# Kernel tuning notes

Hardware: AMD Instinct MI355X
Metric: run time of the kernel (lower is better)

Reference implementation:

```python
import jax, jax.numpy as jnp
import numpy as np

B, NPG = 128, 128          # graphs, nodes per graph
N = B * NPG                # total nodes
K = 16                     # kNN neighbors within cutoff
D = 256                    # embedding_depth
H, DH = 4, 32              # heads = num_layers, head dim = (D//2)//H
L = 4                      # num graph convolutions
NR = 50                    # num_radial
CUTOFF = 2.0
OUT = 3 + 100              # 3 + max_ntypes


def setup_inputs() -> dict:
    rng = np.random.default_rng(0)
    pos = rng.standard_normal((N, 3)).astype(np.float32)
    nbrs = np.zeros((N, K), np.int32)
    mask = np.zeros((N, K), np.float32)
    for g in range(B):  # per-graph kNN with radial cutoff (setup only, numpy)
        p = pos[g * NPG:(g + 1) * NPG]
        d2 = ((p[:, None, :] - p[None, :, :]) ** 2).sum(-1)
        np.fill_diagonal(d2, np.inf)
        idx = np.argsort(d2, axis=1)[:, :K]
        dk = np.sqrt(np.take_along_axis(d2, idx, 1))
        nbrs[g * NPG:(g + 1) * NPG] = idx + g * NPG
        mask[g * NPG:(g + 1) * NPG] = (dk <= CUTOFF).astype(np.float32)
    batch_idx = np.repeat(np.arange(B, dtype=np.int32), NPG)

    key = jax.random.key(0)
    ks = jax.random.split(key, 12)
    s = 0.02
    return {
        'encoding': jax.random.normal(ks[0], (B, D), jnp.float32),
        'pos': jnp.asarray(pos),
        'batch_idx': jnp.asarray(batch_idx),
        'neighbors': jnp.asarray(nbrs),
        'nbr_mask': jnp.asarray(mask),
        'W_in': jax.random.normal(ks[1], (D + 3, D), jnp.float32) * s,
        'b_in': jnp.zeros((D,), jnp.float32),
        'Wq': jax.random.normal(ks[2], (L, D, H * DH), jnp.float32) * s,
        'Wk': jax.random.normal(ks[3], (L, D, H * DH), jnp.float32) * s,
        'Wv': jax.random.normal(ks[4], (L, D, H * DH), jnp.float32) * s,
        'We': jax.random.normal(ks[5], (L, NR, H * DH), jnp.float32) * s,
        'Wo': jax.random.normal(ks[6], (L, H * DH, D), jnp.float32) * s,
        'bo': jnp.zeros((L, D), jnp.float32),
        'Wfc': jax.random.normal(ks[7], (L, D, D), jnp.float32) * s,
        'bfc': jnp.zeros((L, D), jnp.float32),
        'ln_g': jnp.ones((L, D), jnp.float32),
        'ln_b': jnp.zeros((L, D), jnp.float32),
        'W_out': jax.random.normal(ks[8], (D, OUT), jnp.float32) * s,
        'b_out': jnp.zeros((OUT,), jnp.float32),
    }


def reference(encoding, pos, batch_idx, neighbors, nbr_mask,
              W_in, b_in, Wq, Wk, Wv, We, Wo, bo, Wfc, bfc,
              ln_g, ln_b, W_out, b_out):
    # x = encoding.repeat_interleave(graph_sizes); x[:, 0] = 1
    x = encoding[batch_idx]                      # [N, D]
    x = x.at[:, 0].set(1.0)
    h = jnp.concatenate([x, pos], axis=-1) @ W_in + b_in   # concat pos, embed

    # gaussian radial basis of neighbor distances
    dvec = pos[neighbors] - pos[:, None, :]      # [N, K, 3]
    d = jnp.sqrt((dvec ** 2).sum(-1) + 1e-12)    # [N, K]
    centers = jnp.linspace(0.0, CUTOFF, NR)
    width = centers[1] - centers[0]
    rbf = jnp.exp(-0.5 * ((d[..., None] - centers) / width) ** 2)  # [N, K, NR]

    scale = 1.0 / jnp.sqrt(jnp.float32(DH))
    m = nbr_mask[..., None]                      # [N, K, 1]
    for l in range(L):                           # TransformerConv layers
        q = (h @ Wq[l]).reshape(N, H, DH)
        k = (h @ Wk[l]).reshape(N, H, DH)
        v = (h @ Wv[l]).reshape(N, H, DH)
        e = (rbf @ We[l]).reshape(N, K, H, DH)   # edge embedding
        kj = k[neighbors] + e                    # [N, K, H, DH]
        vj = v[neighbors] + e
        logits = jnp.einsum('nhd,nkhd->nkh', q, kj) * scale
        logits = jnp.where(m > 0, logits, -1e9)
        a = jax.nn.softmax(logits, axis=1) * m   # masked attention over K
        msg = jnp.einsum('nkh,nkhd->nhd', a, vj).reshape(N, H * DH)
        h = h + msg @ Wo[l] + bo[l]              # residual update
        mu = h.mean(-1, keepdims=True)
        var = h.var(-1, keepdims=True)
        h = ln_g[l] * (h - mu) / jnp.sqrt(var + 1e-5) + ln_b[l]
        h = jax.nn.gelu(h @ Wfc[l] + bfc[l])     # nodewise fc (1 layer)

    return h @ W_out + b_out                     # [N, 3 + max_ntypes]
```

## Files before the change

### kernel.cpp

```cpp
#include <hip/hip_runtime.h>
#include <hip/hip_bf16.h>
#include <math.h>

#define N_PTS 16384
#define NLAYER 4

typedef __attribute__((ext_vector_type(8))) short bfrag;
typedef __attribute__((ext_vector_type(4))) float f32x4;
typedef unsigned short ushort_t;
typedef unsigned int uint_t;

__device__ __forceinline__ ushort_t f2b(float f) {
  __hip_bfloat16 h = __float2bfloat16(f);
  return *reinterpret_cast<const ushort_t*>(&h);
}
__device__ __forceinline__ float b2f(ushort_t u) {
  union { uint_t i; float f; } c; c.i = ((uint_t)u) << 16; return c.f;
}
__device__ __forceinline__ float blo(uint_t u) {
  union { uint_t i; float f; } c; c.i = u << 16; return c.f;
}
__device__ __forceinline__ float bhi(uint_t u) {
  union { uint_t i; float f; } c; c.i = u & 0xffff0000u; return c.f;
}

__global__ __launch_bounds__(256) void base_kernel(
    const float* __restrict__ enc, const float* __restrict__ W_in,
    const float* __restrict__ b_in, float* __restrict__ base)
{
  int b = blockIdx.x, j = threadIdx.x;
  __shared__ float se[256];
  se[j] = enc[b * 256 + j];
  __syncthreads();
  float acc = b_in[j] + W_in[j];
  for (int i = 1; i < 256; ++i) acc += se[i] * W_in[i * 256 + j];
  base[b * 256 + j] = acc;
}

__global__ __launch_bounds__(256) void embed_kernel(
    const float* __restrict__ base, const int* __restrict__ batch_idx,
    const float* __restrict__ pos, const float* __restrict__ W_in,
    float* __restrict__ h, ushort_t* __restrict__ h_bf)
{
  int n = blockIdx.x, j = threadIdx.x;
  int b = batch_idx[n];
  float px = pos[n * 3 + 0], py = pos[n * 3 + 1], pz = pos[n * 3 + 2];
  float v = base[b * 256 + j]
      + px * W_in[256 * 256 + j] + py * W_in[257 * 256 + j] + pz * W_in[258 * 256 + j];
  h[(size_t)n * 256 + j] = v;
  h_bf[(size_t)n * 256 + j] = f2b(v);
}

__global__ __launch_bounds__(256) void prep_qkv(
    const float* __restrict__ Wq, const float* __restrict__ Wk,
    const float* __restrict__ Wv, const float* __restrict__ We,
    ushort_t* __restrict__ out)
{
  int idx = blockIdx.x * 256 + threadIdx.x;
  int l = idx / (640 * 256);
  int rem = idx - l * (640 * 256);
  int j = rem >> 8, k = rem & 255;
  float v = 0.f;
  if (j < 128) v = Wq[((size_t)l * 256 + k) * 128 + j];
  else if (j < 328) {
    int p = j - 128, hq = p / 50, r = p - hq * 50;
    const float* wq = &Wq[((size_t)l * 256 + k) * 128 + hq * 32];
    const float* we = &We[((size_t)l * 50 + r) * 128 + hq * 32];
#pragma unroll
    for (int d = 0; d < 32; ++d) v += wq[d] * we[d];
  } else if (j < 456) v = Wk[((size_t)l * 256 + k) * 128 + (j - 328)];
  else if (j < 584) v = Wv[((size_t)l * 256 + k) * 128 + (j - 456)];
  out[idx] = f2b(v);
}

__global__ __launch_bounds__(256) void prep_bcat(
    const float* __restrict__ We, const float* __restrict__ Wo, ushort_t* __restrict__ out)
{
  int idx = blockIdx.x * 256 + threadIdx.x;
  int l = idx / (256 * 384);
  int rem = idx - l * (256 * 384);
  int j = rem / 384, k2 = rem - j * 384;
  float v = 0.f;
  if (k2 < 128) v = Wo[((size_t)l * 128 + k2) * 256 + j];
  else if (k2 < 328) {
    int p = k2 - 128, hq = p / 50, r = p - hq * 50;
    const float* we = &We[((size_t)l * 50 + r) * 128 + hq * 32];
    const float* wo = &Wo[((size_t)l * 128 + hq * 32) * 256 + j];
#pragma unroll
    for (int d = 0; d < 32; ++d) v += we[d] * wo[(size_t)d * 256];
  }
  out[idx] = f2b(v);
}

__global__ __launch_bounds__(256) void prep_wfc(
    const float* __restrict__ Wfc, ushort_t* __restrict__ out)
{
  int idx = blockIdx.x * 256 + threadIdx.x;
  int l = idx >> 16, rem = idx & 65535;
  int j = rem >> 8, k = rem & 255;
  out[idx] = f2b(Wfc[((size_t)l * 256 + k) * 256 + j]);
}

__global__ __launch_bounds__(256) void prep_wout(
    const float* __restrict__ W_out, ushort_t* __restrict__ out)
{
  int idx = blockIdx.x * 256 + threadIdx.x;
  int j = idx >> 8, k = idx & 255;
  out[idx] = (j < 103) ? f2b(W_out[(size_t)k * 103 + j]) : (ushort_t)0;
}

template<int MODE>
__global__ __launch_bounds__(512, 4) void fused_layer(
    const ushort_t* __restrict__ A0,
    const ushort_t* __restrict__ BcT,
    const float* __restrict__ bo,
    float* __restrict__ h,
    const float* __restrict__ lg, const float* __restrict__ lb,
    const ushort_t* __restrict__ WfT,
    const float* __restrict__ bfc,
    const ushort_t* __restrict__ W3T,
    const float* __restrict__ b3,
    ushort_t* __restrict__ qext_b, ushort_t* __restrict__ kvb,
    float* __restrict__ outF)
{
  __shared__ __align__(16) ushort_t sA[32 * 384];
  __shared__ __align__(16) ushort_t sH[32 * 256];
  __shared__ float pS[8][32], pSS[8][32];

  const int tid = threadIdx.x;
  const int lane = tid & 63, w = tid >> 6;
  const int l15 = lane & 15, l4 = lane >> 4;
  const int m0 = blockIdx.x * 32;
  const int r7 = l15 & 7;

  f32x4 acc[2][2];

  if constexpr (MODE != 2) {
    for (int i = tid; i < 32 * 48; i += 512) {
      int r = i / 48, c8 = i - r * 48;
      uint4 v = (uint4){0, 0, 0, 0};
      if (c8 < 44) v = *(const uint4*)(A0 + (size_t)(m0 + r) * 352 + c8 * 8);
      *(uint4*)(&sA[r * 384 + ((c8 ^ (r & 7)) << 3)]) = v;
    }
    __syncthreads();

#pragma unroll
    for (int m = 0; m < 2; ++m) {
      acc[m][0] = (f32x4){0.f, 0.f, 0.f, 0.f};
      acc[m][1] = (f32x4){0.f, 0.f, 0.f, 0.f};
    }
    {
      const ushort_t* bB0 = BcT + (size_t)(w * 32 + l15) * 384 + l4 * 8;
      const ushort_t* bB1 = bB0 + 16 * 384;
#pragma unroll
      for (int k0 = 0; k0 < 352; k0 += 32) {
        const int ch = (k0 >> 3) + l4;
        bfrag a0 = *(const bfrag*)(sA + (0 * 16 + l15) * 384 + ((ch ^ r7) << 3));
        bfrag a1 = *(const bfrag*)(sA + (1 * 16 + l15) * 384 + ((ch ^ r7) << 3));
        bfrag b0 = *(const bfrag*)(bB0 + k0);
        bfrag b1 = *(const bfrag*)(bB1 + k0);
        acc[0][0] = __builtin_amdgcn_mfma_f32_16x16x32_bf16(a0, b0, acc[0][0], 0, 0, 0);
        acc[0][1] = __builtin_amdgcn_mfma_f32_16x16x32_bf16(a0, b1, acc[0][1], 0, 0, 0);
        acc[1][0] = __builtin_amdgcn_mfma_f32_16x16x32_bf16(a1, b0, acc[1][0], 0, 0, 0);
        acc[1][1] = __builtin_amdgcn_mfma_f32_16x16x32_bf16(a1, b1, acc[1][1], 0, 0, 0);
      }
    }

    const int c0 = w * 32 + l15, c1 = c0 + 16;
    {
      const float bo0 = bo[c0], bo1 = bo[c1];
#pragma unroll
      for (int m = 0; m < 2; ++m)
#pragma unroll
        for (int i = 0; i < 4; ++i) {
          const int rl = m * 16 + l4 * 4 + i;
          const size_t r = (size_t)(m0 + rl);
          float x0 = acc[m][0][i] + bo0 + h[r * 256 + c0];
          float x1 = acc[m][1][i] + bo1 + h[r * 256 + c1];
          acc[m][0][i] = x0; acc[m][1][i] = x1;
          float s = x0 + x1, ss = x0 * x0 + x1 * x1;
          s += __shfl_xor(s, 1, 64); ss += __shfl_xor(ss, 1, 64);
          s += __shfl_xor(s, 2, 64); ss += __shfl_xor(ss, 2, 64);
          s += __shfl_xor(s, 4, 64); ss += __shfl_xor(ss, 4, 64);
          s += __shfl_xor(s, 8, 64); ss += __shfl_xor(ss, 8, 64);
          if (l15 == 0) { pS[w][rl] = s; pSS[w][rl] = ss; }
        }
    }
    __syncthreads();
    {
      const float g0 = lg[c0], g1 = lg[c1];
      const float b0 = lb[c0], b1 = lb[c1];
      const int ch0 = c0 >> 3, ch1 = c1 >> 3;
#pragma unroll
      for (int m = 0; m < 2; ++m)
#pragma unroll
        for (int i = 0; i < 4; ++i) {
          const int rl = m * 16 + l4 * 4 + i;
          float s = 0.f, ss = 0.f;
#pragma unroll
          for (int w2 = 0; w2 < 8; ++w2) { s += pS[w2][rl]; ss += pSS[w2][rl]; }
          float mu = s * (1.f / 256.f);
          float var = ss * (1.f / 256.f) - mu * mu;
          float inv = 1.0f / sqrtf(var + 1e-5f);
          sH[rl * 256 + (((ch0 ^ (rl & 7)) << 3) | (c0 & 7))] =
              f2b(g0 * (acc[m][0][i] - mu) * inv + b0);
          sH[rl * 256 + (((ch1 ^ (rl & 7)) << 3) | (c1 & 7))] =
              f2b(g1 * (acc[m][1][i] - mu) * inv + b1);
        }
    }
    __syncthreads();

#pragma unroll
    for (int m = 0; m < 2; ++m) {
      acc[m][0] = (f32x4){0.f, 0.f, 0.f, 0.f};
      acc[m][1] = (f32x4){0.f, 0.f, 0.f, 0.f};
    }
    {
      const ushort_t* bB0 = WfT + (size_t)(w * 32 + l15) * 256 + l4 * 8;
      const ushort_t* bB1 = bB0 + 16 * 256;
#pragma unroll
      for (int k0 = 0; k0 < 256; k0 += 32) {
        const int ch = (k0 >> 3) + l4;
        bfrag a0 = *(const bfrag*)(sH + (0 * 16 + l15) * 256 + ((ch ^ r7) << 3));
        bfrag a1 = *(const bfrag*)(sH + (1 * 16 + l15) * 256 + ((ch ^ r7) << 3));
        bfrag b0 = *(const bfrag*)(bB0 + k0);
        bfrag b1 = *(const bfrag*)(bB1 + k0);
        acc[0][0] = __builtin_amdgcn_mfma_f32_16x16x32_bf16(a0, b0, acc[0][0], 0, 0, 0);
        acc[0][1] = __builtin_amdgcn_mfma_f32_16x16x32_bf16(a0, b1, acc[0][1], 0, 0, 0);
        acc[1][0] = __builtin_amdgcn_mfma_f32_16x16x32_bf16(a1, b0, acc[1][0], 0, 0, 0);
        acc[1][1] = __builtin_amdgcn_mfma_f32_16x16x32_bf16(a1, b1, acc[1][1], 0, 0, 0);
      }
    }

    {
      const float bf0 = bfc[c0], bf1 = bfc[c1];
      const int ch0 = c0 >> 3, ch1 = c1 >> 3;
#pragma unroll
      for (int m = 0; m < 2; ++m)
#pragma unroll
        for (int i = 0; i < 4; ++i) {
          const int rl = m * 16 + l4 * 4 + i;
          const size_t r = (size_t)(m0 + rl);
          float x0 = acc[m][0][i] + bf0;
          float x1 = acc[m][1][i] + bf1;
          float t0 = tanhf(0.7978845608028654f * (x0 + 0.044715f * x0 * x0 * x0));
          float t1 = tanhf(0.7978845608028654f * (x1 + 0.044715f * x1 * x1 * x1));
          float gl0 = 0.5f * x0 * (1.f + t0);
          float gl1 = 0.5f * x1 * (1.f + t1);
          h[r * 256 + c0] = gl0;
          h[r * 256 + c1] = gl1;
          sA[rl * 256 + (((ch0 ^ (rl & 7)) << 3) | (c0 & 7))] = f2b(gl0);
          sA[rl * 256 + (((ch1 ^ (rl & 7)) << 3) | (c1 & 7))] = f2b(gl1);
        }
    }
    __syncthreads();
  } else {
    for (int i = tid; i < 32 * 32; i += 512) {
      int r = i >> 5, c8 = i & 31;
      *(uint4*)(&sA[r * 256 + ((c8 ^ (r & 7)) << 3)]) =
          *(const uint4*)(A0 + (size_t)(m0 + r) * 256 + c8 * 8);
    }
    __syncthreads();
  }

  const int NB = (MODE == 1) ? 1 : 5;
  for (int nb = 0; nb < NB; ++nb) {
    f32x4 a3[2];
    a3[0] = (f32x4){0.f, 0.f, 0.f, 0.f};
    a3[1] = (f32x4){0.f, 0.f, 0.f, 0.f};
    const ushort_t* bB = W3T + (size_t)(nb * 128 + w * 16 + l15) * 256 + l4 * 8;
#pragma unroll
    for (int k0 = 0; k0 < 256; k0 += 32) {
      const int ch = (k0 >> 3) + l4;
      bfrag a0 = *(const bfrag*)(sA + (0 * 16 + l15) * 256 + ((ch ^ r7) << 3));
      bfrag a1 = *(const bfrag*)(sA + (1 * 16 + l15) * 256 + ((ch ^ r7) << 3));
      bfrag b0 = *(const bfrag*)(bB + k0);
      a3[0] = __builtin_amdgcn_mfma_f32_16x16x32_bf16(a0, b0, a3[0], 0, 0, 0);
      a3[1] = __builtin_amdgcn_mfma_f32_16x16x32_bf16(a1, b0, a3[1], 0, 0, 0);
    }
    const int c = nb * 128 + w * 16 + l15;
#pragma unroll
    for (int m = 0; m < 2; ++m)
#pragma unroll
      for (int i = 0; i < 4; ++i) {
        const size_t r = (size_t)(m0 + m * 16 + l4 * 4 + i);
        float v = a3[m][i];
        if constexpr (MODE == 1) {
          if (c < 103) outF[r * 103 + c] = v + b3[c];
        } else {
          if (c < 328) qext_b[r * 352 + c] = f2b(v);
          else if (c < 584) kvb[r * 256 + (c - 328)] = f2b(v);
        }
      }
  }
}

__global__ __launch_bounds__(256) void attn_kernel(
    const ushort_t* __restrict__ qext, const ushort_t* __restrict__ kvb,
    const float* __restrict__ pos, const int* __restrict__ nbrs,
    const float* __restrict__ mask, ushort_t* __restrict__ Amsg)
{
  __shared__ __align__(16) ushort_t sQ[4][128];
  __shared__ __align__(16) float    sQE[4][4][52];
  __shared__ __align__(16) ushort_t sRbf[4][16][52];
  __shared__ float sA[4][64];
  __shared__ float sD[4][16];
  __shared__ float sMk[4][16];
  __shared__ int   sNb[4][16];

  const int tid = threadIdx.x;
  const int lane = tid & 63, w = tid >> 6;
  const int g = blockIdx.x & 127, q4 = blockIdx.x >> 7;
  const int kk = lane >> 2, hh = lane & 3;

  for (int it = 0; it < 4; ++it) {
    const int n = g * 128 + q4 * 16 + w * 4 + it;
    if (lane < 16) {
      int nb = nbrs[n * 16 + lane];
      sNb[w][lane] = nb;
      sMk[w][lane] = mask[n * 16 + lane];
      float dx = pos[nb * 3 + 0] - pos[n * 3 + 0];
      float dy = pos[nb * 3 + 1] - pos[n * 3 + 1];
      float dz = pos[nb * 3 + 2] - pos[n * 3 + 2];
      sD[w][lane] = sqrtf(dx * dx + dy * dy + dz * dz + 1e-12f);
      sRbf[w][lane][50] = 0; sRbf[w][lane][51] = 0;
      *(uint4*)(&sQ[w][lane * 8]) = *(const uint4*)(qext + (size_t)n * 352 + lane * 8);
    }
    if (lane < 50) {
      uint2 u = *(const uint2*)(qext + (size_t)n * 352 + 128 + lane * 4);
      int p = lane * 4;
#pragma unroll
      for (int e = 0; e < 4; ++e) {
        ushort_t bb = ((const ushort_t*)&u)[e];
        int pp = p + e, h2 = pp / 50, r = pp - h2 * 50;
        sQE[w][h2][r] = b2f(bb);
      }
    }
    if (lane < 8) sQE[w][lane >> 1][50 + (lane & 1)] = 0.f;
    {
      int kk2 = lane & 15;
      float dk = sD[w][kk2];
      int r0 = lane >> 4;
#pragma unroll
      for (int j = 0; j < 13; ++j) {
        int r = r0 + j * 4;
// ... 64 lines not shown
      }
      uint_t o = (uint_t)f2b(m0v) | ((uint_t)f2b(m1v) << 16);
      *(uint_t*)(&Amsg[(size_t)n * 352 + lane * 2]) = o;
    }
    if (lane < 24) Amsg[(size_t)n * 352 + 328 + lane] = 0;
  }
}

extern "C" void kernel_launch(void* const* d_in, const int* in_sizes, int n_in,
                              void* d_out, int out_size, void* d_ws, size_t ws_size,
                              hipStream_t stream) {
  const float* enc    = (const float*)d_in[0];
  const float* pos    = (const float*)d_in[1];
  const int*   bidx   = (const int*)  d_in[2];
  const int*   nbrs   = (const int*)  d_in[3];
  const float* mask   = (const float*)d_in[4];
  const float* W_in   = (const float*)d_in[5];
  const float* b_in   = (const float*)d_in[6];
  const float* Wq     = (const float*)d_in[7];
  const float* Wk     = (const float*)d_in[8];
  const float* Wv     = (const float*)d_in[9];
  const float* We     = (const float*)d_in[10];
  const float* Wo     = (const float*)d_in[11];
  const float* bo     = (const float*)d_in[12];
  const float* Wfc    = (const float*)d_in[13];
  const float* bfc    = (const float*)d_in[14];
  const float* ln_g   = (const float*)d_in[15];
  const float* ln_b   = (const float*)d_in[16];
  const float* W_out  = (const float*)d_in[17];
  const float* b_out  = (const float*)d_in[18];
  float* out = (float*)d_out;

  const int N = N_PTS;
  float* ws = (float*)d_ws;
  float*    h      = ws;
  ushort_t* qext_b = (ushort_t*)(h + (size_t)N * 256);
  ushort_t* kvb    = qext_b + (size_t)N * 352;
  ushort_t* h_bf   = kvb + (size_t)N * 256;
  ushort_t* Amsg   = h_bf + (size_t)N * 256;
  float*    base   = (float*)(Amsg + (size_t)N * 352);
  ushort_t* WqkvT  = (ushort_t*)(base + 128 * 256);
  ushort_t* BcT    = WqkvT + 4 * 640 * 256;
  ushort_t* WfT    = BcT  + 4 * 256 * 384;
  ushort_t* WoT    = WfT  + 4 * 256 * 256;

  base_kernel<<<128, 256, 0, stream>>>(enc, W_in, b_in, base);
  embed_kernel<<<N, 256, 0, stream>>>(base, bidx, pos, W_in, h, h_bf);
  prep_qkv<<<(4 * 640 * 256) / 256, 256, 0, stream>>>(Wq, Wk, Wv, We, WqkvT);
  prep_bcat<<<(4 * 256 * 384) / 256, 256, 0, stream>>>(We, Wo, BcT);
  prep_wfc<<<(4 * 256 * 256) / 256, 256, 0, stream>>>(Wfc, WfT);
  prep_wout<<<(128 * 256) / 256, 256, 0, stream>>>(W_out, WoT);

  fused_layer<2><<<N / 32, 512, 0, stream>>>(
      h_bf, nullptr, nullptr, nullptr, nullptr, nullptr, nullptr, nullptr,
      WqkvT, nullptr, qext_b, kvb, nullptr);

  for (int l = 0; l < NLAYER; ++l) {
    const ushort_t* BcT_l = BcT + (size_t)l * 256 * 384;
    const ushort_t* WfT_l = WfT + (size_t)l * 256 * 256;
    const float* bo_l  = bo  + (size_t)l * 256;
    const float* bfc_l = bfc + (size_t)l * 256;
    const float* lg_l  = ln_g + (size_t)l * 256;
    const float* lb_l  = ln_b + (size_t)l * 256;

    attn_kernel<<<1024, 256, 0, stream>>>(qext_b, kvb, pos, nbrs, mask, Amsg);

    if (l < NLAYER - 1) {
      const ushort_t* Wqkv_next = WqkvT + (size_t)(l + 1) * 640 * 256;
      fused_layer<0><<<N / 32, 512, 0, stream>>>(
          Amsg, BcT_l, bo_l, h, lg_l, lb_l, WfT_l, bfc_l,
          Wqkv_next, nullptr, qext_b, kvb, nullptr);
    } else {
      fused_layer<1><<<N / 32, 512, 0, stream>>>(
          Amsg, BcT_l, bo_l, h, lg_l, lb_l, WfT_l, bfc_l,
          WoT, b_out, nullptr, nullptr, out);
    }
  }
}
```

Before: 330.3 us.

## Halve fused_layer block to 4 waves with wider per-wave column tiles

```diff
diff --git a/kernel.cpp b/kernel.cpp
--- a/kernel.cpp
+++ b/kernel.cpp
@@ -110,7 +110,7 @@
 }
 
 template<int MODE>
-__global__ __launch_bounds__(512, 4) void fused_layer(
+__global__ __launch_bounds__(256, 3) void fused_layer(
     const ushort_t* __restrict__ A0,
     const ushort_t* __restrict__ BcT,
     const float* __restrict__ bo,
@@ -123,62 +123,72 @@
     ushort_t* __restrict__ qext_b, ushort_t* __restrict__ kvb,
     float* __restrict__ outF)
 {
-  __shared__ __align__(16) ushort_t sA[32 * 384];
-  __shared__ __align__(16) ushort_t sH[32 * 256];
-  __shared__ float pS[8][32], pSS[8][32];
+  __shared__ __align__(16) ushort_t sA[32 * 392];
+  __shared__ __align__(16) ushort_t sH[32 * 264];
+  __shared__ float pS[4][32], pSS[4][32];
 
   const int tid = threadIdx.x;
   const int lane = tid & 63, w = tid >> 6;
   const int l15 = lane & 15, l4 = lane >> 4;
   const int m0 = blockIdx.x * 32;
-  const int r7 = l15 & 7;
-
-  f32x4 acc[2][2];
 
   if constexpr (MODE != 2) {
-    for (int i = tid; i < 32 * 48; i += 512) {
-      int r = i / 48, c8 = i - r * 48;
-      uint4 v = (uint4){0, 0, 0, 0};
-      if (c8 < 44) v = *(const uint4*)(A0 + (size_t)(m0 + r) * 352 + c8 * 8);
-      *(uint4*)(&sA[r * 384 + ((c8 ^ (r & 7)) << 3)]) = v;
+    for (int i = tid; i < 32 * 44; i += 256) {
+      int r = i / 44, c8 = i - r * 44;
+      *(uint4*)(&sA[r * 392 + c8 * 8]) =
+          *(const uint4*)(A0 + (size_t)(m0 + r) * 352 + c8 * 8);
     }
     __syncthreads();
 
-#pragma unroll
-    for (int m = 0; m < 2; ++m) {
-      acc[m][0] = (f32x4){0.f, 0.f, 0.f, 0.f};
-      acc[m][1] = (f32x4){0.f, 0.f, 0.f, 0.f};
-    }
-    {
-      const ushort_t* bB0 = BcT + (size_t)(w * 32 + l15) * 384 + l4 * 8;
-      const ushort_t* bB1 = bB0 + 16 * 384;
+    const int c_0 = w * 64 + l15, c_1 = c_0 + 16, c_2 = c_0 + 32, c_3 = c_0 + 48;
+
+    f32x4 acc[2][4];
+#pragma unroll
+    for (int m = 0; m < 2; ++m)
+#pragma unroll
+      for (int nn = 0; nn < 4; ++nn) acc[m][nn] = (f32x4){0.f, 0.f, 0.f, 0.f};
+    {
+      const ushort_t* bp0 = BcT + (size_t)(c_0) * 384 + l4 * 8;
+      const ushort_t* bp1 = BcT + (size_t)(c_1) * 384 + l4 * 8;
+      const ushort_t* bp2 = BcT + (size_t)(c_2) * 384 + l4 * 8;
+      const ushort_t* bp3 = BcT + (size_t)(c_3) * 384 + l4 * 8;
 #pragma unroll
       for (int k0 = 0; k0 < 352; k0 += 32) {
-        const int ch = (k0 >> 3) + l4;
-        bfrag a0 = *(const bfrag*)(sA + (0 * 16 + l15) * 384 + ((ch ^ r7) << 3));
-        bfrag a1 = *(const bfrag*)(sA + (1 * 16 + l15) * 384 + ((ch ^ r7) << 3));
-        bfrag b0 = *(const bfrag*)(bB0 + k0);
-        bfrag b1 = *(const bfrag*)(bB1 + k0);
+        bfrag a0 = *(const bfrag*)(sA + l15 * 392 + k0 + l4 * 8);
+        bfrag a1 = *(const bfrag*)(sA + (16 + l15) * 392 + k0 + l4 * 8);
+        bfrag b0 = *(const bfrag*)(bp0 + k0);
+        bfrag b1 = *(const bfrag*)(bp1 + k0);
+        bfrag b2 = *(const bfrag*)(bp2 + k0);
+        bfrag b3v = *(const bfrag*)(bp3 + k0);
+        __builtin_amdgcn_s_setprio(1);
         acc[0][0] = __builtin_amdgcn_mfma_f32_16x16x32_bf16(a0, b0, acc[0][0], 0, 0, 0);
         acc[0][1] = __builtin_amdgcn_mfma_f32_16x16x32_bf16(a0, b1, acc[0][1], 0, 0, 0);
+        acc[0][2] = __builtin_amdgcn_mfma_f32_16x16x32_bf16(a0, b2, acc[0][2], 0, 0, 0);
+        acc[0][3] = __builtin_amdgcn_mfma_f32_16x16x32_bf16(a0, b3v, acc[0][3], 0, 0, 0);
         acc[1][0] = __builtin_amdgcn_mfma_f32_16x16x32_bf16(a1, b0, acc[1][0], 0, 0, 0);
         acc[1][1] = __builtin_amdgcn_mfma_f32_16x16x32_bf16(a1, b1, acc[1][1], 0, 0, 0);
-      }
-    }
-
-    const int c0 = w * 32 + l15, c1 = c0 + 16;
-    {
-      const float bo0 = bo[c0], bo1 = bo[c1];
+        acc[1][2] = __builtin_amdgcn_mfma_f32_16x16x32_bf16(a1, b2, acc[1][2], 0, 0, 0);
+        acc[1][3] = __builtin_amdgcn_mfma_f32_16x16x32_bf16(a1, b3v, acc[1][3], 0, 0, 0);
+        __builtin_amdgcn_s_setprio(0);
+      }
+    }
+
+    {
+      const float bo_[4] = {bo[c_0], bo[c_1], bo[c_2], bo[c_3]};
 #pragma unroll
       for (int m = 0; m < 2; ++m)
 #pragma unroll
         for (int i = 0; i < 4; ++i) {
           const int rl = m * 16 + l4 * 4 + i;
           const size_t r = (size_t)(m0 + rl);
-          float x0 = acc[m][0][i] + bo0 + h[r * 256 + c0];
-          float x1 = acc[m][1][i] + bo1 + h[r * 256 + c1];
+          float x0 = acc[m][0][i] + bo_[0] + h[r * 256 + c_0];
+          float x1 = acc[m][1][i] + bo_[1] + h[r * 256 + c_1];
+          float x2 = acc[m][2][i] + bo_[2] + h[r * 256 + c_2];
+          float x3 = acc[m][3][i] + bo_[3] + h[r * 256 + c_3];
           acc[m][0][i] = x0; acc[m][1][i] = x1;
-          float s = x0 + x1, ss = x0 * x0 + x1 * x1;
+          acc[m][2][i] = x2; acc[m][3][i] = x3;
+          float s = x0 + x1 + x2 + x3;
+          float ss = x0 * x0 + x1 * x1 + x2 * x2 + x3 * x3;
           s += __shfl_xor(s, 1, 64); ss += __shfl_xor(ss, 1, 64);
           s += __shfl_xor(s, 2, 64); ss += __shfl_xor(ss, 2, 64);
           s += __shfl_xor(s, 4, 64); ss += __shfl_xor(ss, 4, 64);
@@ -188,103 +198,120 @@
     }
     __syncthreads();
     {
-      const float g0 = lg[c0], g1 = lg[c1];
-      const float b0 = lb[c0], b1 = lb[c1];
-      const int ch0 = c0 >> 3, ch1 = c1 >> 3;
+      const float lg_[4] = {lg[c_0], lg[c_1], lg[c_2], lg[c_3]};
+      const float lb_[4] = {lb[c_0], lb[c_1], lb[c_2], lb[c_3]};
 #pragma unroll
       for (int m = 0; m < 2; ++m)
 #pragma unroll
         for (int i = 0; i < 4; ++i) {
           const int rl = m * 16 + l4 * 4 + i;
-          float s = 0.f, ss = 0.f;
-#pragma unroll
-          for (int w2 = 0; w2 < 8; ++w2) { s += pS[w2][rl]; ss += pSS[w2][rl]; }
+          float s = pS[0][rl] + pS[1][rl] + pS[2][rl] + pS[3][rl];
+          float ss = pSS[0][rl] + pSS[1][rl] + pSS[2][rl] + pSS[3][rl];
           float mu = s * (1.f / 256.f);
           float var = ss * (1.f / 256.f) - mu * mu;
           float inv = 1.0f / sqrtf(var + 1e-5f);
-          sH[rl * 256 + (((ch0 ^ (rl & 7)) << 3) | (c0 & 7))] =
-              f2b(g0 * (acc[m][0][i] - mu) * inv + b0);
-          sH[rl * 256 + (((ch1 ^ (rl & 7)) << 3) | (c1 & 7))] =
-              f2b(g1 * (acc[m][1][i] - mu) * inv + b1);
+          sH[rl * 264 + c_0] = f2b(lg_[0] * (acc[m][0][i] - mu) * inv + lb_[0]);
+          sH[rl * 264 + c_1] = f2b(lg_[1] * (acc[m][1][i] - mu) * inv + lb_[1]);
+          sH[rl * 264 + c_2] = f2b(lg_[2] * (acc[m][2][i] - mu) * inv + lb_[2]);
+          sH[rl * 264 + c_3] = f2b(lg_[3] * (acc[m][3][i] - mu) * inv + lb_[3]);
         }
     }
     __syncthreads();
 
 #pragma unroll
-    for (int m = 0; m < 2; ++m) {
-      acc[m][0] = (f32x4){0.f, 0.f, 0.f, 0.f};
-      acc[m][1] = (f32x4){0.f, 0.f, 0.f, 0.f};
-    }
-    {
-      const ushort_t* bB0 = WfT + (size_t)(w * 32 + l15) * 256 + l4 * 8;
-      const ushort_t* bB1 = bB0 + 16 * 256;
+    for (int m = 0; m < 2; ++m)
+#pragma unroll
+      for (int nn = 0; nn < 4; ++nn) acc[m][nn] = (f32x4){0.f, 0.f, 0.f, 0.f};
+    {
+      const ushort_t* bp0 = WfT + (size_t)(c_0) * 256 + l4 * 8;
+      const ushort_t* bp1 = WfT + (size_t)(c_1) * 256 + l4 * 8;
+      const ushort_t* bp2 = WfT + (size_t)(c_2) * 256 + l4 * 8;
+      const ushort_t* bp3 = WfT + (size_t)(c_3) * 256 + l4 * 8;
 #pragma unroll
       for (int k0 = 0; k0 < 256; k0 += 32) {
-        const int ch = (k0 >> 3) + l4;
-        bfrag a0 = *(const bfrag*)(sH + (0 * 16 + l15) * 256 + ((ch ^ r7) << 3));
-        bfrag a1 = *(const bfrag*)(sH + (1 * 16 + l15) * 256 + ((ch ^ r7) << 3));
-        bfrag b0 = *(const bfrag*)(bB0 + k0);
-        bfrag b1 = *(const bfrag*)(bB1 + k0);
+        bfrag a0 = *(const bfrag*)(sH + l15 * 264 + k0 + l4 * 8);
+        bfrag a1 = *(const bfrag*)(sH + (16 + l15) * 264 + k0 + l4 * 8);
+        bfrag b0 = *(const bfrag*)(bp0 + k0);
+        bfrag b1 = *(const bfrag*)(bp1 + k0);
+        bfrag b2 = *(const bfrag*)(bp2 + k0);
+        bfrag b3v = *(const bfrag*)(bp3 + k0);
+        __builtin_amdgcn_s_setprio(1);
         acc[0][0] = __builtin_amdgcn_mfma_f32_16x16x32_bf16(a0, b0, acc[0][0], 0, 0, 0);
         acc[0][1] = __builtin_amdgcn_mfma_f32_16x16x32_bf16(a0, b1, acc[0][1], 0, 0, 0);
+        acc[0][2] = __builtin_amdgcn_mfma_f32_16x16x32_bf16(a0, b2, acc[0][2], 0, 0, 0);
+        acc[0][3] = __builtin_amdgcn_mfma_f32_16x16x32_bf16(a0, b3v, acc[0][3], 0, 0, 0);
         acc[1][0] = __builtin_amdgcn_mfma_f32_16x16x32_bf16(a1, b0, acc[1][0], 0, 0, 0);
         acc[1][1] = __builtin_amdgcn_mfma_f32_16x16x32_bf16(a1, b1, acc[1][1], 0, 0, 0);
-      }
-    }
-
-    {
-      const float bf0 = bfc[c0], bf1 = bfc[c1];
-      const int ch0 = c0 >> 3, ch1 = c1 >> 3;
+        acc[1][2] = __builtin_amdgcn_mfma_f32_16x16x32_bf16(a1, b2, acc[1][2], 0, 0, 0);
+        acc[1][3] = __builtin_amdgcn_mfma_f32_16x16x32_bf16(a1, b3v, acc[1][3], 0, 0, 0);
+        __builtin_amdgcn_s_setprio(0);
+      }
+    }
+
+    {
+      const float bf_[4] = {bfc[c_0], bfc[c_1], bfc[c_2], bfc[c_3]};
+      const int cc[4] = {c_0, c_1, c_2, c_3};
 #pragma unroll
       for (int m = 0; m < 2; ++m)
 #pragma unroll
         for (int i = 0; i < 4; ++i) {
           const int rl = m * 16 + l4 * 4 + i;
           const size_t r = (size_t)(m0 + rl);
-          float x0 = acc[m][0][i] + bf0;
-          float x1 = acc[m][1][i] + bf1;
-          float t0 = tanhf(0.7978845608028654f * (x0 + 0.044715f * x0 * x0 * x0));
-          float t1 = tanhf(0.7978845608028654f * (x1 + 0.044715f * x1 * x1 * x1));
-          float gl0 = 0.5f * x0 * (1.f + t0);
-          float gl1 = 0.5f * x1 * (1.f + t1);
-          h[r * 256 + c0] = gl0;
-          h[r * 256 + c1] = gl1;
-          sA[rl * 256 + (((ch0 ^ (rl & 7)) << 3) | (c0 & 7))] = f2b(gl0);
-          sA[rl * 256 + (((ch1 ^ (rl & 7)) << 3) | (c1 & 7))] = f2b(gl1);
+#pragma unroll
+          for (int nn = 0; nn < 4; ++nn) {
+            float x = acc[m][nn][i] + bf_[nn];
+            float t = tanhf(0.7978845608028654f * (x + 0.044715f * x * x * x));
+            float gl = 0.5f * x * (1.f + t);
+            h[r * 256 + cc[nn]] = gl;
+            sA[rl * 264 + cc[nn]] = f2b(gl);
+          }
         }
     }
     __syncthreads();
   } else {
-    for (int i = tid; i < 32 * 32; i += 512) {
+    for (int i = tid; i < 32 * 32; i += 256) {
       int r = i >> 5, c8 = i & 31;
-      *(uint4*)(&sA[r * 256 + ((c8 ^ (r & 7)) << 3)]) =
+      *(uint4*)(&sA[r * 264 + c8 * 8]) =
           *(const uint4*)(A0 + (size_t)(m0 + r) * 256 + c8 * 8);
     }
     __syncthreads();
   }
 
-  const int NB = (MODE == 1) ? 1 : 5;
-  for (int nb = 0; nb < NB; ++nb) {
-    f32x4 a3[2];
-    a3[0] = (f32x4){0.f, 0.f, 0.f, 0.f};
-    a3[1] = (f32x4){0.f, 0.f, 0.f, 0.f};
-    const ushort_t* bB = W3T + (size_t)(nb * 128 + w * 16 + l15) * 256 + l4 * 8;
-#pragma unroll
-    for (int k0 = 0; k0 < 256; k0 += 32) {
-      const int ch = (k0 >> 3) + l4;
-      bfrag a0 = *(const bfrag*)(sA + (0 * 16 + l15) * 256 + ((ch ^ r7) << 3));
-      bfrag a1 = *(const bfrag*)(sA + (1 * 16 + l15) * 256 + ((ch ^ r7) << 3));
-      bfrag b0 = *(const bfrag*)(bB + k0);
-      a3[0] = __builtin_amdgcn_mfma_f32_16x16x32_bf16(a0, b0, a3[0], 0, 0, 0);
-      a3[1] = __builtin_amdgcn_mfma_f32_16x16x32_bf16(a1, b0, a3[1], 0, 0, 0);
-    }
-    const int c = nb * 128 + w * 16 + l15;
+  const int NPAN = (MODE == 1) ? 2 : 10;
+  const int WCOL = (MODE == 1) ? 32 : 160;
+  for (int p = 0; p < NPAN; ++p) {
+    const int cb = w * WCOL + p * 16;
+    const int c = cb + l15;
+    const ushort_t* bp = W3T + (size_t)c * 256 + l4 * 8;
+    f32x4 aA[2], aB[2];
+    aA[0] = (f32x4){0.f, 0.f, 0.f, 0.f}; aA[1] = aA[0];
+    aB[0] = aA[0]; aB[1] = aA[0];
+#pragma unroll
+    for (int k0 = 0; k0 < 128; k0 += 32) {
+      bfrag a0 = *(const bfrag*)(sA + l15 * 264 + k0 + l4 * 8);
+      bfrag a1 = *(const bfrag*)(sA + (16 + l15) * 264 + k0 + l4 * 8);
+      bfrag b0 = *(const bfrag*)(bp + k0);
+      __builtin_amdgcn_s_setprio(1);
+      aA[0] = __builtin_amdgcn_mfma_f32_16x16x32_bf16(a0, b0, aA[0], 0, 0, 0);
+      aA[1] = __builtin_amdgcn_mfma_f32_16x16x32_bf16(a1, b0, aA[1], 0, 0, 0);
+      __builtin_amdgcn_s_setprio(0);
+    }
+#pragma unroll
+    for (int k0 = 128; k0 < 256; k0 += 32) {
+      bfrag a0 = *(const bfrag*)(sA + l15 * 264 + k0 + l4 * 8);
+      bfrag a1 = *(const bfrag*)(sA + (16 + l15) * 264 + k0 + l4 * 8);
+      bfrag b0 = *(const bfrag*)(bp + k0);
+      __builtin_amdgcn_s_setprio(1);
+      aB[0] = __builtin_amdgcn_mfma_f32_16x16x32_bf16(a0, b0, aB[0], 0, 0, 0);
+      aB[1] = __builtin_amdgcn_mfma_f32_16x16x32_bf16(a1, b0, aB[1], 0, 0, 0);
+      __builtin_amdgcn_s_setprio(0);
+    }
 #pragma unroll
     for (int m = 0; m < 2; ++m)
 #pragma unroll
       for (int i = 0; i < 4; ++i) {
         const size_t r = (size_t)(m0 + m * 16 + l4 * 4 + i);
-        float v = a3[m][i];
+        float v = aA[m][i] + aB[m][i];
         if constexpr (MODE == 1) {
           if (c < 103) outF[r * 103 + c] = v + b3[c];
         } else {
@@ -460,7 +487,7 @@
   prep_wfc<<<(4 * 256 * 256) / 256, 256, 0, stream>>>(Wfc, WfT);
   prep_wout<<<(128 * 256) / 256, 256, 0, stream>>>(W_out, WoT);
 
-  fused_layer<2><<<N / 32, 512, 0, stream>>>(
+  fused_layer<2><<<N / 32, 256, 0, stream>>>(
       h_bf, nullptr, nullptr, nullptr, nullptr, nullptr, nullptr, nullptr,
       WqkvT, nullptr, qext_b, kvb, nullptr);
 
@@ -476,11 +503,11 @@
 
     if (l < NLAYER - 1) {
       const ushort_t* Wqkv_next = WqkvT + (size_t)(l + 1) * 640 * 256;
-      fused_layer<0><<<N / 32, 512, 0, stream>>>(
+      fused_layer<0><<<N / 32, 256, 0, stream>>>(
           Amsg, BcT_l, bo_l, h, lg_l, lb_l, WfT_l, bfc_l,
           Wqkv_next, nullptr, qext_b, kvb, nullptr);
     } else {
-      fused_layer<1><<<N / 32, 512, 0, stream>>>(
+      fused_layer<1><<<N / 32, 256, 0, stream>>>(
           Amsg, BcT_l, bo_l, h, lg_l, lb_l, WfT_l, bfc_l,
           WoT, b_out, nullptr, nullptr, out);
     }
```

Result: slower. 387.0 us (+17.2%).

## Widen fused layer tile to 64 rows with padded LDS and prefetched weight fragments

Applied to the files above, without the earlier changes.

```diff
diff --git a/kernel.cpp b/kernel.cpp
--- a/kernel.cpp
+++ b/kernel.cpp
@@ -23,6 +23,8 @@
 __device__ __forceinline__ float bhi(uint_t u) {
   union { uint_t i; float f; } c; c.i = u & 0xffff0000u; return c.f;
 }
+
+#define MFMA16(a, b, c) __builtin_amdgcn_mfma_f32_16x16x32_bf16((a), (b), (c), 0, 0, 0)
 
 __global__ __launch_bounds__(256) void base_kernel(
     const float* __restrict__ enc, const float* __restrict__ W_in,
@@ -110,7 +112,7 @@
 }
 
 template<int MODE>
-__global__ __launch_bounds__(512, 4) void fused_layer(
+__global__ __launch_bounds__(512, 1) void fused_layer(
     const ushort_t* __restrict__ A0,
     const ushort_t* __restrict__ BcT,
     const float* __restrict__ bo,
@@ -123,60 +125,71 @@
     ushort_t* __restrict__ qext_b, ushort_t* __restrict__ kvb,
     float* __restrict__ outF)
 {
-  __shared__ __align__(16) ushort_t sA[32 * 384];
-  __shared__ __align__(16) ushort_t sH[32 * 256];
-  __shared__ float pS[8][32], pSS[8][32];
+  __shared__ __align__(16) ushort_t sA[64 * 392];
+  __shared__ __align__(16) ushort_t sH[64 * 264];
+  __shared__ float pS[8][64], pSS[8][64];
 
   const int tid = threadIdx.x;
   const int lane = tid & 63, w = tid >> 6;
   const int l15 = lane & 15, l4 = lane >> 4;
-  const int m0 = blockIdx.x * 32;
-  const int r7 = l15 & 7;
-
-  f32x4 acc[2][2];
+  const int m0 = blockIdx.x * 64;
 
   if constexpr (MODE != 2) {
-    for (int i = tid; i < 32 * 48; i += 512) {
-      int r = i / 48, c8 = i - r * 48;
-      uint4 v = (uint4){0, 0, 0, 0};
-      if (c8 < 44) v = *(const uint4*)(A0 + (size_t)(m0 + r) * 352 + c8 * 8);
-      *(uint4*)(&sA[r * 384 + ((c8 ^ (r & 7)) << 3)]) = v;
+    for (int i = tid; i < 64 * 44; i += 512) {
+      int r = i / 44, c8 = i - r * 44;
+      *(uint4*)(&sA[r * 392 + c8 * 8]) =
+          *(const uint4*)(A0 + (size_t)(m0 + r) * 352 + c8 * 8);
     }
     __syncthreads();
 
-#pragma unroll
-    for (int m = 0; m < 2; ++m) {
+    const int c_0 = w * 32 + l15, c_1 = c_0 + 16;
+
+    f32x4 acc[4][2];
+#pragma unroll
+    for (int m = 0; m < 4; ++m) {
       acc[m][0] = (f32x4){0.f, 0.f, 0.f, 0.f};
       acc[m][1] = (f32x4){0.f, 0.f, 0.f, 0.f};
     }
     {
-      const ushort_t* bB0 = BcT + (size_t)(w * 32 + l15) * 384 + l4 * 8;
-      const ushort_t* bB1 = bB0 + 16 * 384;
+      const ushort_t* bp0 = BcT + (size_t)c_0 * 384 + l4 * 8;
+      const ushort_t* bp1 = BcT + (size_t)c_1 * 384 + l4 * 8;
+      bfrag bc0 = *(const bfrag*)(bp0);
+      bfrag bc1 = *(const bfrag*)(bp1);
 #pragma unroll
       for (int k0 = 0; k0 < 352; k0 += 32) {
-        const int ch = (k0 >> 3) + l4;
-        bfrag a0 = *(const bfrag*)(sA + (0 * 16 + l15) * 384 + ((ch ^ r7) << 3));
-        bfrag a1 = *(const bfrag*)(sA + (1 * 16 + l15) * 384 + ((ch ^ r7) << 3));
-        bfrag b0 = *(const bfrag*)(bB0 + k0);
-        bfrag b1 = *(const bfrag*)(bB1 + k0);
-        acc[0][0] = __builtin_amdgcn_mfma_f32_16x16x32_bf16(a0, b0, acc[0][0], 0, 0, 0);
-        acc[0][1] = __builtin_amdgcn_mfma_f32_16x16x32_bf16(a0, b1, acc[0][1], 0, 0, 0);
-        acc[1][0] = __builtin_amdgcn_mfma_f32_16x16x32_bf16(a1, b0, acc[1][0], 0, 0, 0);
-        acc[1][1] = __builtin_amdgcn_mfma_f32_16x16x32_bf16(a1, b1, acc[1][1], 0, 0, 0);
-      }
-    }
-
-    const int c0 = w * 32 + l15, c1 = c0 + 16;
-    {
-      const float bo0 = bo[c0], bo1 = bo[c1];
-#pragma unroll
-      for (int m = 0; m < 2; ++m)
+        bfrag bn0 = bc0, bn1 = bc1;
+        if (k0 + 32 < 352) {
+          bn0 = *(const bfrag*)(bp0 + k0 + 32);
+          bn1 = *(const bfrag*)(bp1 + k0 + 32);
+        }
+        bfrag a0 = *(const bfrag*)(sA + (l15) * 392 + k0 + l4 * 8);
+        bfrag a1 = *(const bfrag*)(sA + (16 + l15) * 392 + k0 + l4 * 8);
+        bfrag a2 = *(const bfrag*)(sA + (32 + l15) * 392 + k0 + l4 * 8);
+        bfrag a3v = *(const bfrag*)(sA + (48 + l15) * 392 + k0 + l4 * 8);
+        __builtin_amdgcn_s_setprio(1);
+        acc[0][0] = MFMA16(a0, bc0, acc[0][0]);
+        acc[0][1] = MFMA16(a0, bc1, acc[0][1]);
+        acc[1][0] = MFMA16(a1, bc0, acc[1][0]);
+        acc[1][1] = MFMA16(a1, bc1, acc[1][1]);
+        acc[2][0] = MFMA16(a2, bc0, acc[2][0]);
+        acc[2][1] = MFMA16(a2, bc1, acc[2][1]);
+        acc[3][0] = MFMA16(a3v, bc0, acc[3][0]);
+        acc[3][1] = MFMA16(a3v, bc1, acc[3][1]);
+        __builtin_amdgcn_s_setprio(0);
+        bc0 = bn0; bc1 = bn1;
+      }
+    }
+
+    {
+      const float bo0 = bo[c_0], bo1 = bo[c_1];
+#pragma unroll
+      for (int m = 0; m < 4; ++m)
 #pragma unroll
         for (int i = 0; i < 4; ++i) {
           const int rl = m * 16 + l4 * 4 + i;
           const size_t r = (size_t)(m0 + rl);
-          float x0 = acc[m][0][i] + bo0 + h[r * 256 + c0];
-          float x1 = acc[m][1][i] + bo1 + h[r * 256 + c1];
+          float x0 = acc[m][0][i] + bo0 + h[r * 256 + c_0];
+          float x1 = acc[m][1][i] + bo1 + h[r * 256 + c_1];
           acc[m][0][i] = x0; acc[m][1][i] = x1;
           float s = x0 + x1, ss = x0 * x0 + x1 * x1;
           s += __shfl_xor(s, 1, 64); ss += __shfl_xor(ss, 1, 64);
@@ -188,11 +201,10 @@
     }
     __syncthreads();
     {
-      const float g0 = lg[c0], g1 = lg[c1];
-      const float b0 = lb[c0], b1 = lb[c1];
-      const int ch0 = c0 >> 3, ch1 = c1 >> 3;
-#pragma unroll
-      for (int m = 0; m < 2; ++m)
+      const float g0 = lg[c_0], g1 = lg[c_1];
+      const float b0 = lb[c_0], b1 = lb[c_1];
+#pragma unroll
+      for (int m = 0; m < 4; ++m)
 #pragma unroll
         for (int i = 0; i < 4; ++i) {
           const int rl = m * 16 + l4 * 4 + i;
@@ -202,41 +214,51 @@
           float mu = s * (1.f / 256.f);
           float var = ss * (1.f / 256.f) - mu * mu;
           float inv = 1.0f / sqrtf(var + 1e-5f);
-          sH[rl * 256 + (((ch0 ^ (rl & 7)) << 3) | (c0 & 7))] =
-              f2b(g0 * (acc[m][0][i] - mu) * inv + b0);
-          sH[rl * 256 + (((ch1 ^ (rl & 7)) << 3) | (c1 & 7))] =
-              f2b(g1 * (acc[m][1][i] - mu) * inv + b1);
+          sH[rl * 264 + c_0] = f2b(g0 * (acc[m][0][i] - mu) * inv + b0);
+          sH[rl * 264 + c_1] = f2b(g1 * (acc[m][1][i] - mu) * inv + b1);
         }
     }
     __syncthreads();
 
 #pragma unroll
-    for (int m = 0; m < 2; ++m) {
+    for (int m = 0; m < 4; ++m) {
       acc[m][0] = (f32x4){0.f, 0.f, 0.f, 0.f};
       acc[m][1] = (f32x4){0.f, 0.f, 0.f, 0.f};
     }
     {
-      const ushort_t* bB0 = WfT + (size_t)(w * 32 + l15) * 256 + l4 * 8;
-      const ushort_t* bB1 = bB0 + 16 * 256;
+      const ushort_t* bp0 = WfT + (size_t)c_0 * 256 + l4 * 8;
+      const ushort_t* bp1 = WfT + (size_t)c_1 * 256 + l4 * 8;
+      bfrag bc0 = *(const bfrag*)(bp0);
+      bfrag bc1 = *(const bfrag*)(bp1);
 #pragma unroll
       for (int k0 = 0; k0 < 256; k0 += 32) {
-        const int ch = (k0 >> 3) + l4;
-        bfrag a0 = *(const bfrag*)(sH + (0 * 16 + l15) * 256 + ((ch ^ r7) << 3));
-        bfrag a1 = *(const bfrag*)(sH + (1 * 16 + l15) * 256 + ((ch ^ r7) << 3));
-        bfrag b0 = *(const bfrag*)(bB0 + k0);
-        bfrag b1 = *(const bfrag*)(bB1 + k0);
-        acc[0][0] = __builtin_amdgcn_mfma_f32_16x16x32_bf16(a0, b0, acc[0][0], 0, 0, 0);
-        acc[0][1] = __builtin_amdgcn_mfma_f32_16x16x32_bf16(a0, b1, acc[0][1], 0, 0, 0);
-        acc[1][0] = __builtin_amdgcn_mfma_f32_16x16x32_bf16(a1, b0, acc[1][0], 0, 0, 0);
-        acc[1][1] = __builtin_amdgcn_mfma_f32_16x16x32_bf16(a1, b1, acc[1][1], 0, 0, 0);
-      }
-    }
-
-    {
-      const float bf0 = bfc[c0], bf1 = bfc[c1];
-      const int ch0 = c0 >> 3, ch1 = c1 >> 3;
-#pragma unroll
-      for (int m = 0; m < 2; ++m)
+        bfrag bn0 = bc0, bn1 = bc1;
+        if (k0 + 32 < 256) {
+          bn0 = *(const bfrag*)(bp0 + k0 + 32);
+          bn1 = *(const bfrag*)(bp1 + k0 + 32);
+        }
+        bfrag a0 = *(const bfrag*)(sH + (l15) * 264 + k0 + l4 * 8);
+        bfrag a1 = *(const bfrag*)(sH + (16 + l15) * 264 + k0 + l4 * 8);
+        bfrag a2 = *(const bfrag*)(sH + (32 + l15) * 264 + k0 + l4 * 8);
+        bfrag a3v = *(const bfrag*)(sH + (48 + l15) * 264 + k0 + l4 * 8);
+        __builtin_amdgcn_s_setprio(1);
+        acc[0][0] = MFMA16(a0, bc0, acc[0][0]);
+        acc[0][1] = MFMA16(a0, bc1, acc[0][1]);
+        acc[1][0] = MFMA16(a1, bc0, acc[1][0]);
+        acc[1][1] = MFMA16(a1, bc1, acc[1][1]);
+        acc[2][0] = MFMA16(a2, bc0, acc[2][0]);
+        acc[2][1] = MFMA16(a2, bc1, acc[2][1]);
+        acc[3][0] = MFMA16(a3v, bc0, acc[3][0]);
+        acc[3][1] = MFMA16(a3v, bc1, acc[3][1]);
+        __builtin_amdgcn_s_setprio(0);
+        bc0 = bn0; bc1 = bn1;
+      }
+    }
+
+    {
+      const float bf0 = bfc[c_0], bf1 = bfc[c_1];
+#pragma unroll
+      for (int m = 0; m < 4; ++m)
 #pragma unroll
         for (int i = 0; i < 4; ++i) {
           const int rl = m * 16 + l4 * 4 + i;
@@ -247,51 +269,68 @@
           float t1 = tanhf(0.7978845608028654f * (x1 + 0.044715f * x1 * x1 * x1));
           float gl0 = 0.5f * x0 * (1.f + t0);
           float gl1 = 0.5f * x1 * (1.f + t1);
-          h[r * 256 + c0] = gl0;
-          h[r * 256 + c1] = gl1;
-          sA[rl * 256 + (((ch0 ^ (rl & 7)) << 3) | (c0 & 7))] = f2b(gl0);
-          sA[rl * 256 + (((ch1 ^ (rl & 7)) << 3) | (c1 & 7))] = f2b(gl1);
+          h[r * 256 + c_0] = gl0;
+          h[r * 256 + c_1] = gl1;
+          sA[rl * 264 + c_0] = f2b(gl0);
+          sA[rl * 264 + c_1] = f2b(gl1);
         }
     }
     __syncthreads();
   } else {
-    for (int i = tid; i < 32 * 32; i += 512) {
+    for (int i = tid; i < 64 * 32; i += 512) {
       int r = i >> 5, c8 = i & 31;
-      *(uint4*)(&sA[r * 256 + ((c8 ^ (r & 7)) << 3)]) =
+      *(uint4*)(&sA[r * 264 + c8 * 8]) =
           *(const uint4*)(A0 + (size_t)(m0 + r) * 256 + c8 * 8);
     }
     __syncthreads();
   }
 
-  const int NB = (MODE == 1) ? 1 : 5;
-  for (int nb = 0; nb < NB; ++nb) {
-    f32x4 a3[2];
-    a3[0] = (f32x4){0.f, 0.f, 0.f, 0.f};
-    a3[1] = (f32x4){0.f, 0.f, 0.f, 0.f};
-    const ushort_t* bB = W3T + (size_t)(nb * 128 + w * 16 + l15) * 256 + l4 * 8;
-#pragma unroll
-    for (int k0 = 0; k0 < 256; k0 += 32) {
-      const int ch = (k0 >> 3) + l4;
-      bfrag a0 = *(const bfrag*)(sA + (0 * 16 + l15) * 256 + ((ch ^ r7) << 3));
-      bfrag a1 = *(const bfrag*)(sA + (1 * 16 + l15) * 256 + ((ch ^ r7) << 3));
-      bfrag b0 = *(const bfrag*)(bB + k0);
-      a3[0] = __builtin_amdgcn_mfma_f32_16x16x32_bf16(a0, b0, a3[0], 0, 0, 0);
-      a3[1] = __builtin_amdgcn_mfma_f32_16x16x32_bf16(a1, b0, a3[1], 0, 0, 0);
-    }
-    const int c = nb * 128 + w * 16 + l15;
-#pragma unroll
-    for (int m = 0; m < 2; ++m)
-#pragma unroll
-      for (int i = 0; i < 4; ++i) {
-        const size_t r = (size_t)(m0 + m * 16 + l4 * 4 + i);
-        float v = a3[m][i];
-        if constexpr (MODE == 1) {
-          if (c < 103) outF[r * 103 + c] = v + b3[c];
-        } else {
-          if (c < 328) qext_b[r * 352 + c] = f2b(v);
-          else if (c < 584) kvb[r * 256 + (c - 328)] = f2b(v);
-        }
-      }
+  {
+    const int NB = (MODE == 1) ? 1 : 5;
+    const int wc = w * 16 + l15;
+    const int NS = NB * 8;
+    f32x4 a3[4];
+#pragma unroll
+    for (int m = 0; m < 4; ++m) a3[m] = (f32x4){0.f, 0.f, 0.f, 0.f};
+    bfrag bc = *(const bfrag*)(W3T + (size_t)wc * 256 + l4 * 8);
+#pragma unroll
+    for (int s = 0; s < ((MODE == 1) ? 8 : 40); ++s) {
+      bfrag bn = bc;
+      if (s + 1 < NS) {
+        int sn = s + 1;
+        bn = *(const bfrag*)(W3T + (size_t)(((sn >> 3) << 7) + wc) * 256
+                             + ((sn & 7) << 5) + l4 * 8);
+      }
+      const int k0 = (s & 7) << 5;
+      bfrag a0 = *(const bfrag*)(sA + (l15) * 264 + k0 + l4 * 8);
+      bfrag a1 = *(const bfrag*)(sA + (16 + l15) * 264 + k0 + l4 * 8);
+      bfrag a2 = *(const bfrag*)(sA + (32 + l15) * 264 + k0 + l4 * 8);
+      bfrag a3v = *(const bfrag*)(sA + (48 + l15) * 264 + k0 + l4 * 8);
+      __builtin_amdgcn_s_setprio(1);
+      a3[0] = MFMA16(a0, bc, a3[0]);
+      a3[1] = MFMA16(a1, bc, a3[1]);
+      a3[2] = MFMA16(a2, bc, a3[2]);
+      a3[3] = MFMA16(a3v, bc, a3[3]);
+      __builtin_amdgcn_s_setprio(0);
+      bc = bn;
+      if ((s & 7) == 7) {
+        const int c = ((s >> 3) << 7) + wc;
+#pragma unroll
+        for (int m = 0; m < 4; ++m)
+#pragma unroll
+          for (int i = 0; i < 4; ++i) {
+            const size_t r = (size_t)(m0 + m * 16 + l4 * 4 + i);
+            float v = a3[m][i];
+            if constexpr (MODE == 1) {
+              if (c < 103) outF[r * 103 + c] = v + b3[c];
+            } else {
+              if (c < 328) qext_b[r * 352 + c] = f2b(v);
+              else if (c < 584) kvb[r * 256 + (c - 328)] = f2b(v);
+            }
+            a3[m][i] = 0.f;
+          }
+      }
+    }
   }
 }
 
@@ -460,7 +499,7 @@
   prep_wfc<<<(4 * 256 * 256) / 256, 256, 0, stream>>>(Wfc, WfT);
   prep_wout<<<(128 * 256) / 256, 256, 0, stream>>>(W_out, WoT);
 
-  fused_layer<2><<<N / 32, 512, 0, stream>>>(
+  fused_layer<2><<<N / 64, 512, 0, stream>>>(
       h_bf, nullptr, nullptr, nullptr, nullptr, nullptr, nullptr, nullptr,
       WqkvT, nullptr, qext_b, kvb, nullptr);
 
@@ -476,11 +515,11 @@
 
     if (l < NLAYER - 1) {
       const ushort_t* Wqkv_next = WqkvT + (size_t)(l + 1) * 640 * 256;
-      fused_layer<0><<<N / 32, 512, 0, stream>>>(
+      fused_layer<0><<<N / 64, 512, 0, stream>>>(
           Amsg, BcT_l, bo_l, h, lg_l, lb_l, WfT_l, bfc_l,
           Wqkv_next, nullptr, qext_b, kvb, nullptr);
     } else {
-      fused_layer<1><<<N / 32, 512, 0, stream>>>(
+      fused_layer<1><<<N / 64, 512, 0, stream>>>(
           Amsg, BcT_l, bo_l, h, lg_l, lb_l, WfT_l, bfc_l,
           WoT, b_out, nullptr, nullptr, out);
     }
```

Result: slower. 341.4 us (+3.3%).

## Store residual stream in bf16 and remap block order for XCD locality

Applied to the files above, without the earlier changes.

```diff
diff --git a/kernel.cpp b/kernel.cpp
--- a/kernel.cpp
+++ b/kernel.cpp
@@ -40,14 +40,13 @@
 __global__ __launch_bounds__(256) void embed_kernel(
     const float* __restrict__ base, const int* __restrict__ batch_idx,
     const float* __restrict__ pos, const float* __restrict__ W_in,
-    float* __restrict__ h, ushort_t* __restrict__ h_bf)
+    ushort_t* __restrict__ h_bf)
 {
   int n = blockIdx.x, j = threadIdx.x;
   int b = batch_idx[n];
   float px = pos[n * 3 + 0], py = pos[n * 3 + 1], pz = pos[n * 3 + 2];
   float v = base[b * 256 + j]
       + px * W_in[256 * 256 + j] + py * W_in[257 * 256 + j] + pz * W_in[258 * 256 + j];
-  h[(size_t)n * 256 + j] = v;
   h_bf[(size_t)n * 256 + j] = f2b(v);
 }
 
@@ -114,7 +113,7 @@
     const ushort_t* __restrict__ A0,
     const ushort_t* __restrict__ BcT,
     const float* __restrict__ bo,
-    float* __restrict__ h,
+    ushort_t* __restrict__ hb,
     const float* __restrict__ lg, const float* __restrict__ lb,
     const ushort_t* __restrict__ WfT,
     const float* __restrict__ bfc,
@@ -128,9 +127,10 @@
   __shared__ float pS[8][32], pSS[8][32];
 
   const int tid = threadIdx.x;
+  const int bid = blockIdx.x;
   const int lane = tid & 63, w = tid >> 6;
   const int l15 = lane & 15, l4 = lane >> 4;
-  const int m0 = blockIdx.x * 32;
+  const int m0 = ((bid & 7) + 8 * ((bid >> 3) & 15)) * 128 + (bid >> 7) * 32;
   const int r7 = l15 & 7;
 
   f32x4 acc[2][2];
@@ -175,8 +175,8 @@
         for (int i = 0; i < 4; ++i) {
           const int rl = m * 16 + l4 * 4 + i;
           const size_t r = (size_t)(m0 + rl);
-          float x0 = acc[m][0][i] + bo0 + h[r * 256 + c0];
-          float x1 = acc[m][1][i] + bo1 + h[r * 256 + c1];
+          float x0 = acc[m][0][i] + bo0 + b2f(hb[r * 256 + c0]);
+          float x1 = acc[m][1][i] + bo1 + b2f(hb[r * 256 + c1]);
           acc[m][0][i] = x0; acc[m][1][i] = x1;
           float s = x0 + x1, ss = x0 * x0 + x1 * x1;
           s += __shfl_xor(s, 1, 64); ss += __shfl_xor(ss, 1, 64);
@@ -247,10 +247,11 @@
           float t1 = tanhf(0.7978845608028654f * (x1 + 0.044715f * x1 * x1 * x1));
           float gl0 = 0.5f * x0 * (1.f + t0);
           float gl1 = 0.5f * x1 * (1.f + t1);
-          h[r * 256 + c0] = gl0;
-          h[r * 256 + c1] = gl1;
-          sA[rl * 256 + (((ch0 ^ (rl & 7)) << 3) | (c0 & 7))] = f2b(gl0);
-          sA[rl * 256 + (((ch1 ^ (rl & 7)) << 3) | (c1 & 7))] = f2b(gl1);
+          ushort_t u0 = f2b(gl0), u1 = f2b(gl1);
+          hb[r * 256 + c0] = u0;
+          hb[r * 256 + c1] = u1;
+          sA[rl * 256 + (((ch0 ^ (rl & 7)) << 3) | (c0 & 7))] = u0;
+          sA[rl * 256 + (((ch1 ^ (rl & 7)) << 3) | (c1 & 7))] = u1;
         }
     }
     __syncthreads();
@@ -309,8 +310,10 @@
   __shared__ int   sNb[4][16];
 
   const int tid = threadIdx.x;
+  const int bid = blockIdx.x;
   const int lane = tid & 63, w = tid >> 6;
-  const int g = blockIdx.x & 127, q4 = blockIdx.x >> 7;
+  const int g = (bid & 7) + 8 * ((bid >> 3) & 15);
+  const int q4 = bid >> 7;
   const int kk = lane >> 2, hh = lane & 3;
 
   for (int it = 0; it < 4; ++it) {
@@ -441,12 +444,11 @@
   float* out = (float*)d_out;
 
   const int N = N_PTS;
-  float* ws = (float*)d_ws;
-  float*    h      = ws;
-  ushort_t* qext_b = (ushort_t*)(h + (size_t)N * 256);
+  ushort_t* ws = (ushort_t*)d_ws;
+  ushort_t* hb     = ws;
+  ushort_t* qext_b = hb + (size_t)N * 256;
   ushort_t* kvb    = qext_b + (size_t)N * 352;
-  ushort_t* h_bf   = kvb + (size_t)N * 256;
-  ushort_t* Amsg   = h_bf + (size_t)N * 256;
+  ushort_t* Amsg   = kvb + (size_t)N * 256;
   float*    base   = (float*)(Amsg + (size_t)N * 352);
   ushort_t* WqkvT  = (ushort_t*)(base + 128 * 256);
   ushort_t* BcT    = WqkvT + 4 * 640 * 256;
@@ -454,14 +456,14 @@
   ushort_t* WoT    = WfT  + 4 * 256 * 256;
 
   base_kernel<<<128, 256, 0, stream>>>(enc, W_in, b_in, base);
-  embed_kernel<<<N, 256, 0, stream>>>(base, bidx, pos, W_in, h, h_bf);
+  embed_kernel<<<N, 256, 0, stream>>>(base, bidx, pos, W_in, hb);
   prep_qkv<<<(4 * 640 * 256) / 256, 256, 0, stream>>>(Wq, Wk, Wv, We, WqkvT);
   prep_bcat<<<(4 * 256 * 384) / 256, 256, 0, stream>>>(We, Wo, BcT);
   prep_wfc<<<(4 * 256 * 256) / 256, 256, 0, stream>>>(Wfc, WfT);
   prep_wout<<<(128 * 256) / 256, 256, 0, stream>>>(W_out, WoT);
 
   fused_layer<2><<<N / 32, 512, 0, stream>>>(
-      h_bf, nullptr, nullptr, nullptr, nullptr, nullptr, nullptr, nullptr,
+      hb, nullptr, nullptr, nullptr, nullptr, nullptr, nullptr, nullptr,
       WqkvT, nullptr, qext_b, kvb, nullptr);
 
   for (int l = 0; l < NLAYER; ++l) {
@@ -477,11 +479,11 @@
     if (l < NLAYER - 1) {
       const ushort_t* Wqkv_next = WqkvT + (size_t)(l + 1) * 640 * 256;
       fused_layer<0><<<N / 32, 512, 0, stream>>>(
-          Amsg, BcT_l, bo_l, h, lg_l, lb_l, WfT_l, bfc_l,
+          Amsg, BcT_l, bo_l, hb, lg_l, lb_l, WfT_l, bfc_l,
           Wqkv_next, nullptr, qext_b, kvb, nullptr);
     } else {
       fused_layer<1><<<N / 32, 512, 0, stream>>>(
-          Amsg, BcT_l, bo_l, h, lg_l, lb_l, WfT_l, bfc_l,
+          Amsg, BcT_l, bo_l, hb, lg_l, lb_l, WfT_l, bfc_l,
           WoT, b_out, nullptr, nullptr, out);
     }
   }
```

After: 328.3 us. Within noise of the previous version (-0.6%).
